# Kernel tuning notes

Hardware: AMD Instinct MI355X
Metric: run time of the kernel (lower is better)

## Reference

```python
import jax, jax.numpy as jnp
import numpy as np

NT, NP = 100000, 20000
FT, FP, H = 128, 64, 128
E, EL = 2000000, 500000
EPS = 1e-12


def _l2norm(x):
    # F.normalize(x, p=2, dim=-1): x / max(||x||, eps)
    n = jnp.sqrt(jnp.sum(x * x, axis=-1, keepdims=True))
    return x / jnp.maximum(n, EPS)


def _seg_mean(x_src, src_idx, dst_idx, n_dst, inv_cnt):
    # gather src features per edge, scatter-sum to dst, divide by in-degree
    s = jax.ops.segment_sum(x_src[src_idx], dst_idx, num_segments=n_dst)
    return s * inv_cnt[:, None]


def setup_inputs() -> dict:
    key = jax.random.key(0)
    ks = jax.random.split(key, 24)

    def w(k, fan_in, fan_out):
        return jax.random.normal(k, (fan_in, fan_out), jnp.float32) / np.sqrt(fan_in)

    inp = {
        "x_track": jax.random.normal(ks[0], (NT, FT), jnp.float32),
        "x_playlist": jax.random.normal(ks[1], (NP, FP), jnp.float32),
        "edge_src": jax.random.randint(ks[2], (E,), 0, NT),
        "edge_dst": jax.random.randint(ks[3], (E,), 0, NP),
        "label_src": jax.random.randint(ks[4], (EL,), 0, NT),
        "label_dst": jax.random.randint(ks[5], (EL,), 0, NP),
        # per-type input projections (PyG Linear, bias=True)
        "Wn_t": w(ks[6], FT, H), "bn_t": jnp.zeros((H,), jnp.float32),
        "Wn_p": w(ks[7], FP, H), "bn_p": jnp.zeros((H,), jnp.float32),
        # layer1: edge type track->playlist (dst playlist) and reverse (dst track)
        "W1_l_p": w(ks[8], H, H), "b1_p": jnp.zeros((H,), jnp.float32), "W1_r_p": w(ks[9], H, H),
        "W1_l_t": w(ks[10], H, H), "b1_t": jnp.zeros((H,), jnp.float32), "W1_r_t": w(ks[11], H, H),
        # layer2
        "W2_l_p": w(ks[12], H, H), "b2_p": jnp.zeros((H,), jnp.float32), "W2_r_p": w(ks[13], H, H),
        "W2_l_t": w(ks[14], H, H), "b2_t": jnp.zeros((H,), jnp.float32), "W2_r_t": w(ks[15], H, H),
    }
    return inp


def reference(x_track, x_playlist, edge_src, edge_dst, label_src, label_dst,
              Wn_t, bn_t, Wn_p, bn_p,
              W1_l_p, b1_p, W1_r_p, W1_l_t, b1_t, W1_r_t,
              W2_l_p, b2_p, W2_r_p, W2_l_t, b2_t, W2_r_t):
    nt, np_ = x_track.shape[0], x_playlist.shape[0]
    ones = jnp.ones(edge_src.shape, jnp.float32)
    inv_cnt_p = 1.0 / jnp.maximum(jax.ops.segment_sum(ones, edge_dst, num_segments=np_), 1.0)
    inv_cnt_t = 1.0 / jnp.maximum(jax.ops.segment_sum(ones, edge_src, num_segments=nt), 1.0)

    # per-type input linear
    h_t = x_track @ Wn_t + bn_t        # [NT, H]
    h_p = x_playlist @ Wn_p + bn_p     # [NP, H]

    # hetero SAGE layer 1 (normalize=True) + relu
    agg_p = _seg_mean(h_t, edge_src, edge_dst, np_, inv_cnt_p)  # track -> playlist
    agg_t = _seg_mean(h_p, edge_dst, edge_src, nt, inv_cnt_t)   # playlist -> track (rev edges)
    o_p = jax.nn.relu(_l2norm(agg_p @ W1_l_p + b1_p + h_p @ W1_r_p))
    o_t = jax.nn.relu(_l2norm(agg_t @ W1_l_t + b1_t + h_t @ W1_r_t))

    # hetero SAGE layer 2 (normalize=True), no relu
    agg_p2 = _seg_mean(o_t, edge_src, edge_dst, np_, inv_cnt_p)
    agg_t2 = _seg_mean(o_p, edge_dst, edge_src, nt, inv_cnt_t)
    z_p = _l2norm(agg_p2 @ W2_l_p + b2_p + o_p @ W2_r_p)
    z_t = _l2norm(agg_t2 @ W2_l_t + b2_t + o_t @ W2_r_t)

    # link predictor: dot product of endpoint embeddings
    return jnp.sum(z_t[label_src] * z_p[label_dst], axis=-1)  # [EL]
```

## Files before the change

kernel.cpp:

```cpp
#include <hip/hip_runtime.h>
#include <hip/hip_bf16.h>

#define H 128

typedef __attribute__((ext_vector_type(8))) _Float16 f16x8;
typedef __attribute__((ext_vector_type(4))) _Float16 f16x4;
typedef __attribute__((ext_vector_type(4))) float f32x4;

static inline size_t align_up(size_t x, size_t a){ return (x + a - 1) & ~(a - 1); }

__device__ inline f32x4 mfma16h(f16x8 a, f16x8 b, f32x4 c){
  return __builtin_amdgcn_mfma_f32_16x16x32_f16(a, b, c, 0, 0, 0);
}

__device__ inline void gload_lds16(const void* g, void* l){
  __builtin_amdgcn_global_load_lds(
      (const __attribute__((address_space(1))) void*)g,
      (__attribute__((address_space(3))) void*)l, 16, 0, 0);
}

__global__ __launch_bounds__(256) void hist_buckets(const int* __restrict__ src, const int* __restrict__ dst,
    int E, int* __restrict__ cnt_b_p, int* __restrict__ cnt_b_t){
  __shared__ int hp[256], ht[256];
  int tid = threadIdx.x;
  hp[tid] = 0; ht[tid] = 0;
  __syncthreads();
  for (int i = blockIdx.x * 256 + tid; i < E; i += gridDim.x * 256){
    atomicAdd(&hp[dst[i] >> 7], 1);
    atomicAdd(&ht[src[i] >> 9], 1);
  }
  __syncthreads();
  if (hp[tid]) atomicAdd(&cnt_b_p[tid], hp[tid]);
  if (ht[tid]) atomicAdd(&cnt_b_t[tid], ht[tid]);
}

__global__ void scan_buckets(const int* __restrict__ cb_p, const int* __restrict__ cb_t, int nbp, int nbt,
                             int* __restrict__ base_p, int* __restrict__ base_t,
                             int* __restrict__ cur_p, int* __restrict__ cur_t){
  if (threadIdx.x == 0){
    int s = 0;
    for (int i = 0; i < nbp; i++){ base_p[i] = s; cur_p[i] = s; s += cb_p[i]; }
    base_p[nbp] = s;
  } else if (threadIdx.x == 1){
    int s = 0;
    for (int i = 0; i < nbt; i++){ base_t[i] = s; cur_t[i] = s; s += cb_t[i]; }
    base_t[nbt] = s;
  }
}

__global__ __launch_bounds__(256) void bin_edges(const int* __restrict__ keys, const int* __restrict__ vals,
    int E, int shift, int nb, int* __restrict__ cursor, unsigned* __restrict__ rec_out){
  const int CH = 4096, IT = 16;
  __shared__ int hist[256];
  __shared__ int excl[256];
  __shared__ int gbase[256];
  __shared__ unsigned recs[CH];
  __shared__ unsigned char binid[CH];
  int tid = threadIdx.x;
  int start = blockIdx.x * CH;
  int cnt = E - start; if (cnt > CH) cnt = CH;
  if (cnt <= 0) return;
  hist[tid] = 0;
  __syncthreads();
  int b[IT]; int rank[IT]; unsigned rc[IT];
  unsigned mask = (1u << shift) - 1u;
  #pragma unroll
  for (int q = 0; q < IT; q++){
    int i = tid + q * 256;
    if (i < cnt){
      int k = keys[start + i], v = vals[start + i];
      b[q] = k >> shift;
      rc[q] = ((unsigned)v << shift) | ((unsigned)k & mask);
      rank[q] = atomicAdd(&hist[b[q]], 1);
    } else b[q] = -1;
  }
  __syncthreads();
  int lane = tid & 63, wid = tid >> 6;
  if (wid == 0){
    int h0 = hist[lane*4], h1 = hist[lane*4+1], h2 = hist[lane*4+2], h3 = hist[lane*4+3];
    int s = h0 + h1 + h2 + h3;
    int sc = s;
    #pragma unroll
    for (int o = 1; o < 64; o <<= 1){ int t = __shfl_up(sc, (unsigned)o, 64); if (lane >= o) sc += t; }
    int base = sc - s;
    excl[lane*4] = base; excl[lane*4+1] = base + h0;
    excl[lane*4+2] = base + h0 + h1; excl[lane*4+3] = base + h0 + h1 + h2;
  }
  __syncthreads();
  #pragma unroll
  for (int q = 0; q < IT; q++){
    if (b[q] >= 0){
      int pos = excl[b[q]] + rank[q];
      recs[pos] = rc[q];
      binid[pos] = (unsigned char)b[q];
    }
  }
  if (tid < nb && hist[tid] > 0) gbase[tid] = atomicAdd(&cursor[tid], hist[tid]);
  __syncthreads();
  for (int i = tid; i < cnt; i += 256){
    int bb = binid[i];
    rec_out[gbase[bb] + (i - excl[bb])] = recs[i];
  }
}

template<int LOC>
__global__ __launch_bounds__(256) void build_csr(const unsigned* __restrict__ rec, const int* __restrict__ bbase,
    int nkeys, int E, int* __restrict__ off, float* __restrict__ inv, int* __restrict__ csr){
  constexpr int LB = (LOC == 128) ? 7 : 9;
  __shared__ int hist[LOC];
  __shared__ int excl[LOC];
  __shared__ int cur[LOC];
  __shared__ int wsum[8];
  int b = blockIdx.x, tid = threadIdx.x;
  int s = bbase[b], e = bbase[b + 1];
  for (int k = tid; k < LOC; k += 256){ hist[k] = 0; cur[k] = 0; }
  __syncthreads();
  for (int i = s + tid; i < e; i += 256) atomicAdd(&hist[rec[i] & (LOC - 1)], 1);
  __syncthreads();
  int lane = tid & 63, wid = tid >> 6;
  constexpr int BPT = (LOC + 255) / 256;
  int h[BPT]; int ssum = 0;
  #pragma unroll
  for (int q = 0; q < BPT; q++){
    int k = tid * BPT + q;
    h[q] = (k < LOC) ? hist[k] : 0;
    ssum += h[q];
  }
  int sc = ssum;
  #pragma unroll
  for (int o = 1; o < 64; o <<= 1){ int t = __shfl_up(sc, (unsigned)o, 64); if (lane >= o) sc += t; }
  if (lane == 63) wsum[wid] = sc;
  __syncthreads();
  int base = 0;
  for (int w = 0; w < wid; w++) base += wsum[w];
  int ex = base + sc - ssum;
  #pragma unroll
  for (int q = 0; q < BPT; q++){
    int k = tid * BPT + q;
    if (k < LOC) excl[k] = ex;
    ex += h[q];
  }
  __syncthreads();
  int keybase = b << LB;
  for (int k = tid; k < LOC; k += 256){
    int gk = keybase + k;
    if (gk < nkeys){
      off[gk] = s + excl[k];
      int c = hist[k];
      inv[gk] = 1.0f / (float)(c > 1 ? c : 1);
    }
  }
  if (b == (int)gridDim.x - 1 && tid == 0) off[nkeys] = E;
  for (int i = s + tid; i < e; i += 256){
    unsigned r = rec[i];
    int k = (int)(r & (LOC - 1));
    int rk = atomicAdd(&cur[k], 1);
    csr[s + excl[k] + rk] = (int)(r >> LB);
  }
}

struct PackArgs {
  const float* src[10];
  _Float16* dst[10];
  int K[10];
  int start[11];
};
__global__ __launch_bounds__(256) void pack_w(PackArgs pa){
  int t = blockIdx.x * 256 + threadIdx.x;
  if (t >= pa.start[10]) return;
  int m = 0;
  #pragma unroll
  for (int i = 1; i < 10; i++) if (t >= pa.start[i]) m = i;
  int local = t - pa.start[m];
  int k = local >> 7, n = local & 127;
  float w = pa.src[m][local];
  _Float16 hi = (_Float16)w;
  _Float16 lo = (_Float16)(w - (float)hi);
  _Float16* d = pa.dst[m];
  int Km = pa.K[m];
  d[n * Km + k] = hi;
  d[128 * Km + n * Km + k] = lo;
}

template<int KA, bool CVT, bool DUAL, bool NORM, bool RELU>
__global__ __launch_bounds__(512) void sage_mfma(
    const void* __restrict__ Ain, const _Float16* __restrict__ Bs,
    const _Float16* __restrict__ WlT, const _Float16* __restrict__ WrT,
    const float* __restrict__ bias, _Float16* __restrict__ OUT, int M, int ntiles)
{
  constexpr int KST = KA / 32;
  constexpr int RB_A = CVT ? KA * 4 : KA * 2;
  constexpr int CHA = RB_A / 16;
  constexpr int NIA = 64 * CHA / 512;
  constexpr int NIB = DUAL ? 2 : 0;
  constexpr int LPI = NIA + NIB;
  constexpr int ABYTES = 64 * RB_A;
  constexpr int BBYTES = DUAL ? 64 * 256 : 0;
  constexpr int BUFB = ABYTES + BBYTES;

  __shared__ __align__(16) char lds[2 * BUFB];
  __shared__ float red[8][64];

  const int t    = threadIdx.x;
  const int wid  = t >> 6;
  const int lane = t & 63;
  const int l15  = lane & 15;
  const int lkg  = lane >> 4;
  const int colg = wid * 16 + l15;

  f16x8 wl_hi[KST], wl_lo[KST];
  {
    const _Float16* bh = WlT + (size_t)colg * KA + lkg * 8;
    #pragma unroll
    for (int ks = 0; ks < KST; ks++){
      wl_hi[ks] = *(const f16x8*)(bh + ks * 32);
      wl_lo[ks] = *(const f16x8*)(bh + 128 * KA + ks * 32);
    }
  }
  f16x8 wr_hi[DUAL ? 4 : 1], wr_lo[DUAL ? 4 : 1];
  if (DUAL){
    const _Float16* bh = WrT + (size_t)colg * 128 + lkg * 8;
    #pragma unroll
    for (int ks = 0; ks < (DUAL ? 4 : 1); ks++){
      wr_hi[ks] = *(const f16x8*)(bh + ks * 32);
      wr_lo[ks] = *(const f16x8*)(bh + 128 * 128 + ks * 32);
    }
  }
  const float bb = bias[colg];

  auto stage = [&](int tile, char* dstA, char* dstB){
    int row0 = tile * 64;
    #pragma unroll
    for (int q = 0; q < NIA; q++){
      int lc  = q * 512 + t;
      int row = lc / CHA;
      int ch  = lc - row * CHA;
      int grow = row0 + row; if (grow > M - 1) grow = M - 1;
      int gch = ch ^ (row & 7);
      gload_lds16((const char*)Ain + (size_t)grow * RB_A + gch * 16, dstA + lc * 16);
    }
    if (DUAL){
      #pragma unroll
      for (int q = 0; q < NIB; q++){
        int lc  = q * 512 + t;
        int row = lc >> 4;
        int ch  = lc & 15;
        int grow = row0 + row; if (grow > M - 1) grow = M - 1;
        int gch = ch ^ (row & 7);
        gload_lds16((const char*)Bs + (size_t)grow * 256 + gch * 16, dstB + lc * 16);
      }
    }
  };

  int p = 0;
  stage(blockIdx.x, lds, lds + ABYTES);

  for (int t0 = blockIdx.x; t0 < ntiles; t0 += gridDim.x){
    const int row0 = t0 * 64;
    const int tn = t0 + (int)gridDim.x;
    const bool hasnext = tn < ntiles;
    if (hasnext) stage(tn, lds + (p ^ 1) * BUFB, lds + (p ^ 1) * BUFB + ABYTES);

    if (hasnext){
      if constexpr (LPI == 4) asm volatile("s_waitcnt vmcnt(4)" ::: "memory");
      else                    asm volatile("s_waitcnt vmcnt(2)" ::: "memory");
    } else {
      asm volatile("s_waitcnt vmcnt(0)" ::: "memory");
    }
    __builtin_amdgcn_s_barrier();
    asm volatile("" ::: "memory");

    const char* bufA = lds + p * BUFB;
    const char* bufB = bufA + ABYTES;

    f32x4 acc[4];
    #pragma unroll
    for (int tt = 0; tt < 4; tt++){
      acc[tt] = (f32x4){0.f, 0.f, 0.f, 0.f};
      const int rl = tt * 16 + l15;
      const int sw = rl & 7;
      if (CVT){
        const char* ap = bufA + rl * RB_A;
        #pragma unroll
        for (int ks = 0; ks < KST; ks++){
          int c0 = lkg * 2 + ks * 8;
          f32x4 a0 = *(const f32x4*)(ap + ((c0    ) ^ sw) * 16);
          f32x4 a1 = *(const f32x4*)(ap + ((c0 + 1) ^ sw) * 16);
          f16x8 af;
          #pragma unroll
          for (int e = 0; e < 8; e++) af[e] = (_Float16)(e < 4 ? a0[e] : a1[e - 4]);
          acc[tt] = mfma16h(af, wl_hi[ks], acc[tt]);
          acc[tt] = mfma16h(af, wl_lo[ks], acc[tt]);
        }
      } else {
        const char* ap = bufA + rl * RB_A;
        #pragma unroll
        for (int ks = 0; ks < KST; ks++){
          f16x8 af = *(const f16x8*)(ap + ((ks * 4 + lkg) ^ sw) * 16);
          acc[tt] = mfma16h(af, wl_hi[ks], acc[tt]);
          acc[tt] = mfma16h(af, wl_lo[ks], acc[tt]);
        }
      }
      if (DUAL){
        const char* bp = bufB + rl * 256;
        #pragma unroll
        for (int ks = 0; ks < 4; ks++){
          f16x8 bf = *(const f16x8*)(bp + ((ks * 4 + lkg) ^ sw) * 16);
          acc[tt] = mfma16h(bf, wr_hi[ks], acc[tt]);
          acc[tt] = mfma16h(bf, wr_lo[ks], acc[tt]);
        }
      }
      acc[tt].x += bb; acc[tt].y += bb; acc[tt].z += bb; acc[tt].w += bb;
    }

    if (NORM){
      #pragma unroll
      for (int tt = 0; tt < 4; tt++){
        #pragma unroll
        for (int r = 0; r < 4; r++){
          float v = acc[tt][r] * acc[tt][r];
          v += __shfl_xor(v, 1, 64);
          v += __shfl_xor(v, 2, 64);
          v += __shfl_xor(v, 4, 64);
          v += __shfl_xor(v, 8, 64);
          if (l15 == 0) red[wid][tt * 16 + lkg * 4 + r] = v;
        }
      }
      asm volatile("s_waitcnt lgkmcnt(0)" ::: "memory");
      __builtin_amdgcn_s_barrier();
      asm volatile("" ::: "memory");
      #pragma unroll
      for (int tt = 0; tt < 4; tt++){
        #pragma unroll
        for (int r = 0; r < 4; r++){
          int idx = tt * 16 + lkg * 4 + r;
          float s = 0.f;
          #pragma unroll
          for (int w2 = 0; w2 < 8; w2++) s += red[w2][idx];
          float scale = 1.f / fmaxf(sqrtf(s), 1e-12f);
          acc[tt][r] *= scale;
        }
      }
    }
    if (RELU){
      #pragma unroll
      for (int tt = 0; tt < 4; tt++){
        acc[tt].x = fmaxf(acc[tt].x, 0.f); acc[tt].y = fmaxf(acc[tt].y, 0.f);
        acc[tt].z = fmaxf(acc[tt].z, 0.f); acc[tt].w = fmaxf(acc[tt].w, 0.f);
      }
    }
    #pragma unroll
    for (int tt = 0; tt < 4; tt++){
      #pragma unroll
      for (int r = 0; r < 4; r++){
        int row = row0 + tt * 16 + lkg * 4 + r;
        if (row < M) OUT[(size_t)row * H + colg] = (_Float16)acc[tt][r];
      }
    }
    if (!NORM){
      asm volatile("s_waitcnt lgkmcnt(0)" ::: "memory");
      __builtin_amdgcn_s_barrier();
      asm volatile("" ::: "memory");
    }
    p ^= 1;
  }
}

struct SageJob {
  const _Float16* A;
  const _Float16* Bs;
  const _Float16* WlT;
  const _Float16* WrT;
  const float* bias;
  _Float16* OUT;
  int M;
  int ntiles;
  int nblk;
};
template<bool RELU>
__global__ __launch_bounds__(512) void sage_mfma2(SageJob j0, SageJob j1){
  constexpr int KST = 4;
  constexpr int RB_A = 256;
  constexpr int CHA = 16;
  constexpr int NIA = 2, NIB = 2;
  constexpr int ABYTES = 64 * 256;
  constexpr int BUFB = 2 * ABYTES;

  __shared__ __align__(16) char lds[2 * BUFB];
  __shared__ float red[8][64];

  const bool second = (int)blockIdx.x >= j0.nblk;
  const SageJob j = second ? j1 : j0;
  const int bid = (int)blockIdx.x - (second ? j0.nblk : 0);
  const int M = j.M, ntiles = j.ntiles, nblk = j.nblk;

  const int t    = threadIdx.x;
  const int wid  = t >> 6;
  const int lane = t & 63;
  const int l15  = lane & 15;
  const int lkg  = lane >> 4;
  const int colg = wid * 16 + l15;

  f16x8 wl_hi[KST], wl_lo[KST], wr_hi[KST], wr_lo[KST];
  {
    const _Float16* bh = j.WlT + (size_t)colg * 128 + lkg * 8;
    const _Float16* bh2 = j.WrT + (size_t)colg * 128 + lkg * 8;
    #pragma unroll
    for (int ks = 0; ks < KST; ks++){
      wl_hi[ks] = *(const f16x8*)(bh + ks * 32);
      wl_lo[ks] = *(const f16x8*)(bh + 128 * 128 + ks * 32);
      wr_hi[ks] = *(const f16x8*)(bh2 + ks * 32);
      wr_lo[ks] = *(const f16x8*)(bh2 + 128 * 128 + ks * 32);
    }
  }
  const float bb = j.bias[colg];

  auto stage = [&](int tile, char* dstA, char* dstB){
    int row0 = tile * 64;
    #pragma unroll
    for (int q = 0; q < NIA; q++){
      int lc  = q * 512 + t;
      int row = lc / CHA;
      int ch  = lc - row * CHA;
      int grow = row0 + row; if (grow > M - 1) grow = M - 1;
      int gch = ch ^ (row & 7);
      gload_lds16((const char*)j.A + (size_t)grow * 256 + gch * 16, dstA + lc * 16);
    }
    #pragma unroll
    for (int q = 0; q < NIB; q++){
      int lc  = q * 512 + t;
      int row = lc >> 4;
      int ch  = lc & 15;
      int grow = row0 + row; if (grow > M - 1) grow = M - 1;
      int gch = ch ^ (row & 7);
      gload_lds16((const char*)j.Bs + (size_t)grow * 256 + gch * 16, dstB + lc * 16);
    }
  };

  int p = 0;
  if (bid < ntiles) stage(bid, lds, lds + ABYTES);

  for (int t0 = bid; t0 < ntiles; t0 += nblk){
    const int row0 = t0 * 64;
    const int tn = t0 + nblk;
    const bool hasnext = tn < ntiles;
    if (hasnext) stage(tn, lds + (p ^ 1) * BUFB, lds + (p ^ 1) * BUFB + ABYTES);

    if (hasnext) asm volatile("s_waitcnt vmcnt(4)" ::: "memory");
    else         asm volatile("s_waitcnt vmcnt(0)" ::: "memory");
    __builtin_amdgcn_s_barrier();
    asm volatile("" ::: "memory");

    const char* bufA = lds + p * BUFB;
    const char* bufB = bufA + ABYTES;

    f32x4 acc[4];
    #pragma unroll
    for (int tt = 0; tt < 4; tt++){
      acc[tt] = (f32x4){0.f, 0.f, 0.f, 0.f};
      const int rl = tt * 16 + l15;
      const int sw = rl & 7;
      const char* ap = bufA + rl * 256;
      #pragma unroll
      for (int ks = 0; ks < KST; ks++){
        f16x8 af = *(const f16x8*)(ap + ((ks * 4 + lkg) ^ sw) * 16);
        acc[tt] = mfma16h(af, wl_hi[ks], acc[tt]);
        acc[tt] = mfma16h(af, wl_lo[ks], acc[tt]);
      }
      const char* bp = bufB + rl * 256;
      #pragma unroll
      for (int ks = 0; ks < KST; ks++){
        f16x8 bf = *(const f16x8*)(bp + ((ks * 4 + lkg) ^ sw) * 16);
        acc[tt] = mfma16h(bf, wr_hi[ks], acc[tt]);
        acc[tt] = mfma16h(bf, wr_lo[ks], acc[tt]);
      }
      acc[tt].x += bb; acc[tt].y += bb; acc[tt].z += bb; acc[tt].w += bb;
    }

    #pragma unroll
    for (int tt = 0; tt < 4; tt++){
      #pragma unroll
      for (int r = 0; r < 4; r++){
        float v = acc[tt][r] * acc[tt][r];
        v += __shfl_xor(v, 1, 64);
        v += __shfl_xor(v, 2, 64);
        v += __shfl_xor(v, 4, 64);
        v += __shfl_xor(v, 8, 64);
        if (l15 == 0) red[wid][tt * 16 + lkg * 4 + r] = v;
      }
    }
    asm volatile("s_waitcnt lgkmcnt(0)" ::: "memory");
    __builtin_amdgcn_s_barrier();
    asm volatile("" ::: "memory");
    #pragma unroll
    for (int tt = 0; tt < 4; tt++){
      #pragma unroll
      for (int r = 0; r < 4; r++){
        int idx = tt * 16 + lkg * 4 + r;
        float s = 0.f;
        #pragma unroll
        for (int w2 = 0; w2 < 8; w2++) s += red[w2][idx];
        float scale = 1.f / fmaxf(sqrtf(s), 1e-12f);
        float v = acc[tt][r] * scale;
        if (RELU) v = fmaxf(v, 0.f);
        acc[tt][r] = v;
      }
    }
    #pragma unroll
    for (int tt = 0; tt < 4; tt++){
      #pragma unroll
      for (int r = 0; r < 4; r++){
        int row = row0 + tt * 16 + lkg * 4 + r;
        if (row < M) j.OUT[(size_t)row * H + colg] = (_Float16)acc[tt][r];
      }
    }
    p ^= 1;
  }
}

struct AggJob {
  const _Float16* feat;
  const int* csr;
  const int* off;
  const float* inv;
  _Float16* out;
  int n;
  int nblk;
};
__global__ __launch_bounds__(256) void agg2_kernel(AggJob j0, AggJob j1){
  const bool second = (int)blockIdx.x >= j0.nblk;
  const AggJob j = second ? j1 : j0;
  const int bid = (int)blockIdx.x - (second ? j0.nblk : 0);
  int g = bid * 16 + (threadIdx.x >> 4);
  int l = threadIdx.x & 15;
  if (g >= j.n) return;
  int s = j.off[g], e = j.off[g + 1];
  float c0[8], c1[8], c2[8], c3[8];
  #pragma unroll
  for (int q = 0; q < 8; q++){ c0[q] = 0.f; c1[q] = 0.f; c2[q] = 0.f; c3[q] = 0.f; }
  const _Float16* F = j.feat;
  int i = s;
  for (; i + 3 < e; i += 4){
    f16x8 v0 = *(const f16x8*)(F + (size_t)j.csr[i]     * H + l * 8);
    f16x8 v1 = *(const f16x8*)(F + (size_t)j.csr[i + 1] * H + l * 8);
    f16x8 v2 = *(const f16x8*)(F + (size_t)j.csr[i + 2] * H + l * 8);
    f16x8 v3 = *(const f16x8*)(F + (size_t)j.csr[i + 3] * H + l * 8);
    #pragma unroll
    for (int q = 0; q < 8; q++){
      c0[q] += (float)v0[q]; c1[q] += (float)v1[q];
      c2[q] += (float)v2[q]; c3[q] += (float)v3[q];
    }
  }
  for (; i < e; i++){
    f16x8 v0 = *(const f16x8*)(F + (size_t)j.csr[i] * H + l * 8);
    #pragma unroll
    for (int q = 0; q < 8; q++) c0[q] += (float)v0[q];
  }
  float iv = j.inv[g];
  f16x8 ov;
  #pragma unroll
  for (int q = 0; q < 8; q++){
    float r = (c0[q] + c1[q]) + (c2[q] + c3[q]);
    ov[q] = (_Float16)(r * iv);
  }
  *(f16x8*)(j.out + (size_t)g * H + l * 8) = ov;
}

__global__ __launch_bounds__(256) void dot_kernel(const _Float16* __restrict__ zt, const _Float16* __restrict__ zp,
                           const int* __restrict__ ls, const int* __restrict__ ld,
                           float* __restrict__ out, int n){
  int w = (blockIdx.x * 256 + threadIdx.x) >> 4;
  int l = threadIdx.x & 15;
  if (w >= n) return;
  f16x8 x = *(const f16x8*)&zt[(size_t)ls[w] * H + l * 8];
  f16x8 y = *(const f16x8*)&zp[(size_t)ld[w] * H + l * 8];
  float v = 0.f;
  #pragma unroll
  for (int q = 0; q < 8; q++) v += (float)x[q] * (float)y[q];
  v += __shfl_xor(v, 1, 64);
  v += __shfl_xor(v, 2, 64);
  v += __shfl_xor(v, 4, 64);
  v += __shfl_xor(v, 8, 64);
  if (l == 0) out[w] = v;
}

extern "C" void kernel_launch(void* const* d_in, const int* in_sizes, int n_in,
                              void* d_out, int out_size, void* d_ws, size_t ws_size,
                              hipStream_t stream){
  const float* x_t  = (const float*)d_in[0];
  const float* x_p  = (const float*)d_in[1];
  const int*   esrc = (const int*)d_in[2];
  const int*   edst = (const int*)d_in[3];
  const int*   lsrc = (const int*)d_in[4];
  const int*   ldst = (const int*)d_in[5];
  const float* Wn_t = (const float*)d_in[6];
  const float* bn_t = (const float*)d_in[7];
  const float* Wn_p = (const float*)d_in[8];
  const float* bn_p = (const float*)d_in[9];
  const float* W1_l_p=(const float*)d_in[10]; const float* b1_p=(const float*)d_in[11]; const float* W1_r_p=(const float*)d_in[12];
  const float* W1_l_t=(const float*)d_in[13]; const float* b1_t=(const float*)d_in[14]; const float* W1_r_t=(const float*)d_in[15];
  const float* W2_l_p=(const float*)d_in[16]; const float* b2_p=(const float*)d_in[17]; const float* W2_r_p=(const float*)d_in[18];
  const float* W2_l_t=(const float*)d_in[19]; const float* b2_t=(const float*)d_in[20]; const float* W2_r_t=(const float*)d_in[21];
  float* out = (float*)d_out;

  const int FT = 128, FP = 64;
  int NT = in_sizes[0] / FT;
  int NP = in_sizes[1] / FP;
  int E  = in_sizes[2];
  int EL = in_sizes[4];

  const int SH_P = 7, SH_T = 9;
  int nb_p = (NP + (1 << SH_P) - 1) >> SH_P;
  int nb_t = (NT + (1 << SH_T) - 1) >> SH_T;

  char* base = (char*)d_ws;
  size_t o = 0;
  auto alloc = [&](size_t bytes) -> char* { char* p = base + o; o = align_up(o + bytes, 256); return p; };
  int*   cb_p  = (int*)alloc(256 * 4);
  int*   cb_t  = (int*)alloc(256 * 4);
  size_t zero_bytes = o;
  int*   bb_p  = (int*)alloc(260 * 4);
  int*   bb_t  = (int*)alloc(260 * 4);
  int*   cu_p  = (int*)alloc(256 * 4);
  int*   cu_t  = (int*)alloc(256 * 4);
  int*   off_p = (int*)alloc((size_t)(NP + 1) * 4);
  int*   off_t = (int*)alloc((size_t)(NT + 1) * 4);
  float* inv_p = (float*)alloc((size_t)NP * 4);
  float* inv_t = (float*)alloc((size_t)NT * 4);
  unsigned* rec_p = (unsigned*)alloc((size_t)E * 4);
  unsigned* rec_t = (unsigned*)alloc((size_t)E * 4);
  int*   csr_p = (int*)alloc((size_t)E * 4);
  int*   csr_t = (int*)alloc((size_t)E * 4);
  _Float16* h_t = (_Float16*)alloc((size_t)NT * H * 2);
  _Float16* h_p = (_Float16*)alloc((size_t)NP * H * 2);
  _Float16* a_t = (_Float16*)alloc((size_t)NT * H * 2);
  _Float16* a_p = (_Float16*)alloc((size_t)NP * H * 2);

  PackArgs pa;
  const float* wsrc[10] = {Wn_t, Wn_p, W1_l_p, W1_r_p, W1_l_t, W1_r_t, W2_l_p, W2_r_p, W2_l_t, W2_r_t};
  int Ks[10] = {128, 64, 128, 128, 128, 128, 128, 128, 128, 128};
  _Float16* wpk[10];
  int st = 0;
  for (int m = 0; m < 10; m++){
    wpk[m] = (_Float16*)alloc((size_t)2 * 128 * Ks[m] * 2);
    pa.src[m] = wsrc[m]; pa.dst[m] = wpk[m]; pa.K[m] = Ks[m]; pa.start[m] = st;
    st += Ks[m] * 128;
  }
  pa.start[10] = st;
  (void)ws_size; (void)n_in; (void)out_size;

  hipMemsetAsync(base, 0, zero_bytes, stream);
  pack_w<<<(st + 255) / 256, 256, 0, stream>>>(pa);

  hist_buckets<<<512, 256, 0, stream>>>(esrc, edst, E, cb_p, cb_t);
  scan_buckets<<<1, 64, 0, stream>>>(cb_p, cb_t, nb_p, nb_t, bb_p, bb_t, cu_p, cu_t);
  int nchunks = (E + 4095) / 4096;
  bin_edges<<<nchunks, 256, 0, stream>>>(edst, esrc, E, SH_P, nb_p, cu_p, rec_p);
  bin_edges<<<nchunks, 256, 0, stream>>>(esrc, edst, E, SH_T, nb_t, cu_t, rec_t);
  build_csr<128><<<nb_p, 256, 0, stream>>>(rec_p, bb_p, NP, E, off_p, inv_p, csr_p);
  build_csr<512><<<nb_t, 256, 0, stream>>>(rec_t, bb_t, NT, E, off_t, inv_t, csr_t);

  int tiles_t = (NT + 63) / 64;
  int tiles_p = (NP + 63) / 64;
  int grid_t = tiles_t < 512 ? tiles_t : 512;
  int grid_p = tiles_p < 512 ? tiles_p : 512;

  sage_mfma<128,true,false,false,false><<<grid_t, 512, 0, stream>>>(x_t, nullptr, wpk[0], nullptr, bn_t, h_t, NT, tiles_t);
  sage_mfma<64, true,false,false,false><<<grid_p, 512, 0, stream>>>(x_p, nullptr, wpk[1], nullptr, bn_p, h_p, NP, tiles_p);

  int ablk_p = (NP + 15) / 16;
  int ablk_t = (NT + 15) / 16;
  AggJob aj_p1{h_t, csr_p, off_p, inv_p, a_p, NP, ablk_p};
  AggJob aj_t1{h_p, csr_t, off_t, inv_t, a_t, NT, ablk_t};
  AggJob aj_p2{a_t, csr_p, off_p, inv_p, h_p, NP, ablk_p};
  AggJob aj_t2{a_p, csr_t, off_t, inv_t, h_t, NT, ablk_t};

  int nblk_p = tiles_p < 96 ? tiles_p : 96;
  int nblk_t = tiles_t < 416 ? tiles_t : 416;
  SageJob sj1p{a_p, h_p, wpk[2], wpk[3], b1_p, a_p, NP, tiles_p, nblk_p};
  SageJob sj1t{a_t, h_t, wpk[4], wpk[5], b1_t, a_t, NT, tiles_t, nblk_t};
  SageJob sj2p{h_p, a_p, wpk[6], wpk[7], b2_p, h_p, NP, tiles_p, nblk_p};
  SageJob sj2t{h_t, a_t, wpk[8], wpk[9], b2_t, h_t, NT, tiles_t, nblk_t};

  agg2_kernel<<<ablk_p + ablk_t, 256, 0, stream>>>(aj_p1, aj_t1);
  sage_mfma2<true><<<nblk_p + nblk_t, 512, 0, stream>>>(sj1p, sj1t);

  agg2_kernel<<<ablk_p + ablk_t, 256, 0, stream>>>(aj_p2, aj_t2);
  sage_mfma2<false><<<nblk_p + nblk_t, 512, 0, stream>>>(sj2p, sj2t);

  dot_kernel<<<(EL + 15) / 16, 256, 0, stream>>>(h_t, h_p, lsrc, ldst, out, EL);
}
```

Baseline: 546.6 us.

## Merge preprocessing and projection kernels into fewer combined launches

```diff
diff --git a/kernel.cpp b/kernel.cpp
--- a/kernel.cpp
+++ b/kernel.cpp
@@ -4,7 +4,6 @@
 #define H 128
 
 typedef __attribute__((ext_vector_type(8))) _Float16 f16x8;
-typedef __attribute__((ext_vector_type(4))) _Float16 f16x4;
 typedef __attribute__((ext_vector_type(4))) float f32x4;
 
 static inline size_t align_up(size_t x, size_t a){ return (x + a - 1) & ~(a - 1); }
@@ -19,19 +18,45 @@
       (__attribute__((address_space(3))) void*)l, 16, 0, 0);
 }
 
-__global__ __launch_bounds__(256) void hist_buckets(const int* __restrict__ src, const int* __restrict__ dst,
-    int E, int* __restrict__ cnt_b_p, int* __restrict__ cnt_b_t){
-  __shared__ int hp[256], ht[256];
-  int tid = threadIdx.x;
-  hp[tid] = 0; ht[tid] = 0;
-  __syncthreads();
-  for (int i = blockIdx.x * 256 + tid; i < E; i += gridDim.x * 256){
-    atomicAdd(&hp[dst[i] >> 7], 1);
-    atomicAdd(&ht[src[i] >> 9], 1);
-  }
-  __syncthreads();
-  if (hp[tid]) atomicAdd(&cnt_b_p[tid], hp[tid]);
-  if (ht[tid]) atomicAdd(&cnt_b_t[tid], ht[tid]);
+struct PackArgs {
+  const float* src[10];
+  _Float16* dst[10];
+  int K[10];
+  int start[11];
+};
+
+__global__ __launch_bounds__(256) void pack_hist(PackArgs pa, int nblk_pack,
+    const int* __restrict__ src, const int* __restrict__ dst, int E,
+    int* __restrict__ cnt_b_p, int* __restrict__ cnt_b_t, int histgrid){
+  if ((int)blockIdx.x < nblk_pack){
+    int t = blockIdx.x * 256 + threadIdx.x;
+    if (t >= pa.start[10]) return;
+    int m = 0;
+    #pragma unroll
+    for (int i = 1; i < 10; i++) if (t >= pa.start[i]) m = i;
+    int local = t - pa.start[m];
+    int k = local >> 7, n = local & 127;
+    float w = pa.src[m][local];
+    _Float16 hi = (_Float16)w;
+    _Float16 lo = (_Float16)(w - (float)hi);
+    _Float16* d = pa.dst[m];
+    int Km = pa.K[m];
+    d[n * Km + k] = hi;
+    d[128 * Km + n * Km + k] = lo;
+  } else {
+    int bid = (int)blockIdx.x - nblk_pack;
+    __shared__ int hp[256], ht[256];
+    int tid = threadIdx.x;
+    hp[tid] = 0; ht[tid] = 0;
+    __syncthreads();
+    for (int i = bid * 256 + tid; i < E; i += histgrid * 256){
+      atomicAdd(&hp[dst[i] >> 7], 1);
+      atomicAdd(&ht[src[i] >> 9], 1);
+    }
+    __syncthreads();
+    if (hp[tid]) atomicAdd(&cnt_b_p[tid], hp[tid]);
+    if (ht[tid]) atomicAdd(&cnt_b_t[tid], ht[tid]);
+  }
 }
 
 __global__ void scan_buckets(const int* __restrict__ cb_p, const int* __restrict__ cb_t, int nbp, int nbt,
@@ -48,16 +73,12 @@
   }
 }
 
-__global__ __launch_bounds__(256) void bin_edges(const int* __restrict__ keys, const int* __restrict__ vals,
-    int E, int shift, int nb, int* __restrict__ cursor, unsigned* __restrict__ rec_out){
+__device__ inline void bin_body(const int* __restrict__ keys, const int* __restrict__ vals,
+    int E, int shift, int nb, int* __restrict__ cursor, unsigned* __restrict__ rec_out, int chunk,
+    int* hist, int* excl, int* gbase, unsigned* recs, unsigned char* binid){
   const int CH = 4096, IT = 16;
-  __shared__ int hist[256];
-  __shared__ int excl[256];
-  __shared__ int gbase[256];
-  __shared__ unsigned recs[CH];
-  __shared__ unsigned char binid[CH];
   int tid = threadIdx.x;
-  int start = blockIdx.x * CH;
+  int start = chunk * CH;
   int cnt = E - start; if (cnt > CH) cnt = CH;
   if (cnt <= 0) return;
   hist[tid] = 0;
@@ -103,15 +124,24 @@
   }
 }
 
-template<int LOC>
-__global__ __launch_bounds__(256) void build_csr(const unsigned* __restrict__ rec, const int* __restrict__ bbase,
-    int nkeys, int E, int* __restrict__ off, float* __restrict__ inv, int* __restrict__ csr){
-  constexpr int LB = (LOC == 128) ? 7 : 9;
-  __shared__ int hist[LOC];
-  __shared__ int excl[LOC];
-  __shared__ int cur[LOC];
-  __shared__ int wsum[8];
-  int b = blockIdx.x, tid = threadIdx.x;
+__global__ __launch_bounds__(256) void bin2(const int* __restrict__ esrc, const int* __restrict__ edst,
+    int E, int nb_p, int* cu_p, unsigned* rec_p, int nb_t, int* cu_t, unsigned* rec_t, int nchunks){
+  __shared__ int hist[256];
+  __shared__ int excl[256];
+  __shared__ int gbase[256];
+  __shared__ unsigned recs[4096];
+  __shared__ unsigned char binid[4096];
+  if ((int)blockIdx.x < nchunks)
+    bin_body(edst, esrc, E, 7, nb_p, cu_p, rec_p, blockIdx.x, hist, excl, gbase, recs, binid);
+  else
+    bin_body(esrc, edst, E, 9, nb_t, cu_t, rec_t, blockIdx.x - nchunks, hist, excl, gbase, recs, binid);
+}
+
+template<int LOC, int LB>
+__device__ inline void build_body(const unsigned* __restrict__ rec, const int* __restrict__ bbase,
+    int nkeys, int E, int* __restrict__ off, float* __restrict__ inv, int* __restrict__ csr,
+    int b, int nb, int* hist, int* excl, int* cur, int* wsum){
+  int tid = threadIdx.x;
   int s = bbase[b], e = bbase[b + 1];
   for (int k = tid; k < LOC; k += 256){ hist[k] = 0; cur[k] = 0; }
   __syncthreads();
@@ -150,7 +180,7 @@
       inv[gk] = 1.0f / (float)(c > 1 ? c : 1);
     }
   }
-  if (b == (int)gridDim.x - 1 && tid == 0) off[nkeys] = E;
+  if (b == nb - 1 && tid == 0) off[nkeys] = E;
   for (int i = s + tid; i < e; i += 256){
     unsigned r = rec[i];
     int k = (int)(r & (LOC - 1));
@@ -159,47 +189,35 @@
   }
 }
 
-struct PackArgs {
-  const float* src[10];
-  _Float16* dst[10];
-  int K[10];
-  int start[11];
+__global__ __launch_bounds__(256) void build2(
+    const unsigned* rec_p, const int* bb_p, int NPk, int* off_p, float* inv_p, int* csr_p, int nb_p,
+    const unsigned* rec_t, const int* bb_t, int NTk, int* off_t, float* inv_t, int* csr_t, int nb_t, int E){
+  __shared__ int hist[512];
+  __shared__ int excl[512];
+  __shared__ int cur[512];
+  __shared__ int wsum[8];
+  if ((int)blockIdx.x < nb_p)
+    build_body<128,7>(rec_p, bb_p, NPk, E, off_p, inv_p, csr_p, blockIdx.x, nb_p, hist, excl, cur, wsum);
+  else
+    build_body<512,9>(rec_t, bb_t, NTk, E, off_t, inv_t, csr_t, blockIdx.x - nb_p, nb_t, hist, excl, cur, wsum);
+}
+
+struct ProjJob {
+  const float* A;
+  const _Float16* WT;
+  const float* bias;
+  _Float16* OUT;
+  int M;
+  int ntiles;
+  int nblk;
 };
-__global__ __launch_bounds__(256) void pack_w(PackArgs pa){
-  int t = blockIdx.x * 256 + threadIdx.x;
-  if (t >= pa.start[10]) return;
-  int m = 0;
-  #pragma unroll
-  for (int i = 1; i < 10; i++) if (t >= pa.start[i]) m = i;
-  int local = t - pa.start[m];
-  int k = local >> 7, n = local & 127;
-  float w = pa.src[m][local];
-  _Float16 hi = (_Float16)w;
-  _Float16 lo = (_Float16)(w - (float)hi);
-  _Float16* d = pa.dst[m];
-  int Km = pa.K[m];
-  d[n * Km + k] = hi;
-  d[128 * Km + n * Km + k] = lo;
-}
-
-template<int KA, bool CVT, bool DUAL, bool NORM, bool RELU>
-__global__ __launch_bounds__(512) void sage_mfma(
-    const void* __restrict__ Ain, const _Float16* __restrict__ Bs,
-    const _Float16* __restrict__ WlT, const _Float16* __restrict__ WrT,
-    const float* __restrict__ bias, _Float16* __restrict__ OUT, int M, int ntiles)
-{
+template<int KA>
+__device__ inline void proj_body(ProjJob j, int bid, char* lds){
   constexpr int KST = KA / 32;
-  constexpr int RB_A = CVT ? KA * 4 : KA * 2;
+  constexpr int RB_A = KA * 4;
   constexpr int CHA = RB_A / 16;
   constexpr int NIA = 64 * CHA / 512;
-  constexpr int NIB = DUAL ? 2 : 0;
-  constexpr int LPI = NIA + NIB;
   constexpr int ABYTES = 64 * RB_A;
-  constexpr int BBYTES = DUAL ? 64 * 256 : 0;
-  constexpr int BUFB = ABYTES + BBYTES;
-
-  __shared__ __align__(16) char lds[2 * BUFB];
-  __shared__ float red[8][64];
 
   const int t    = threadIdx.x;
   const int wid  = t >> 6;
@@ -207,28 +225,20 @@
   const int l15  = lane & 15;
   const int lkg  = lane >> 4;
   const int colg = wid * 16 + l15;
+  const int M = j.M, ntiles = j.ntiles, nblk = j.nblk;
 
   f16x8 wl_hi[KST], wl_lo[KST];
   {
-    const _Float16* bh = WlT + (size_t)colg * KA + lkg * 8;
+    const _Float16* bh = j.WT + (size_t)colg * KA + lkg * 8;
     #pragma unroll
     for (int ks = 0; ks < KST; ks++){
       wl_hi[ks] = *(const f16x8*)(bh + ks * 32);
       wl_lo[ks] = *(const f16x8*)(bh + 128 * KA + ks * 32);
     }
   }
-  f16x8 wr_hi[DUAL ? 4 : 1], wr_lo[DUAL ? 4 : 1];
-  if (DUAL){
-    const _Float16* bh = WrT + (size_t)colg * 128 + lkg * 8;
-    #pragma unroll
-    for (int ks = 0; ks < (DUAL ? 4 : 1); ks++){
-      wr_hi[ks] = *(const f16x8*)(bh + ks * 32);
-      wr_lo[ks] = *(const f16x8*)(bh + 128 * 128 + ks * 32);
-    }
-  }
-  const float bb = bias[colg];
-
-  auto stage = [&](int tile, char* dstA, char* dstB){
+  const float bb = j.bias[colg];
+
+  auto stage = [&](int tile, char* dstA){
     int row0 = tile * 64;
     #pragma unroll
     for (int q = 0; q < NIA; q++){
@@ -237,32 +247,21 @@
       int ch  = lc - row * CHA;
       int grow = row0 + row; if (grow > M - 1) grow = M - 1;
       int gch = ch ^ (row & 7);
-      gload_lds16((const char*)Ain + (size_t)grow * RB_A + gch * 16, dstA + lc * 16);
-    }
-    if (DUAL){
-      #pragma unroll
-      for (int q = 0; q < NIB; q++){
-        int lc  = q * 512 + t;
-        int row = lc >> 4;
-        int ch  = lc & 15;
-        int grow = row0 + row; if (grow > M - 1) grow = M - 1;
-        int gch = ch ^ (row & 7);
-        gload_lds16((const char*)Bs + (size_t)grow * 256 + gch * 16, dstB + lc * 16);
-      }
+      gload_lds16((const char*)j.A + (size_t)grow * RB_A + gch * 16, dstA + lc * 16);
     }
   };
 
   int p = 0;
-  stage(blockIdx.x, lds, lds + ABYTES);
-
-  for (int t0 = blockIdx.x; t0 < ntiles; t0 += gridDim.x){
+  if (bid < ntiles) stage(bid, lds);
+
+  for (int t0 = bid; t0 < ntiles; t0 += nblk){
     const int row0 = t0 * 64;
-    const int tn = t0 + (int)gridDim.x;
+    const int tn = t0 + nblk;
     const bool hasnext = tn < ntiles;
-    if (hasnext) stage(tn, lds + (p ^ 1) * BUFB, lds + (p ^ 1) * BUFB + ABYTES);
+    if (hasnext) stage(tn, lds + (p ^ 1) * ABYTES);
 
     if (hasnext){
-      if constexpr (LPI == 4) asm volatile("s_waitcnt vmcnt(4)" ::: "memory");
+      if constexpr (NIA == 4) asm volatile("s_waitcnt vmcnt(4)" ::: "memory");
       else                    asm volatile("s_waitcnt vmcnt(2)" ::: "memory");
     } else {
       asm volatile("s_waitcnt vmcnt(0)" ::: "memory");
@@ -270,8 +269,7 @@
     __builtin_amdgcn_s_barrier();
     asm volatile("" ::: "memory");
 
-    const char* bufA = lds + p * BUFB;
-    const char* bufB = bufA + ABYTES;
+    const char* bufA = lds + p * ABYTES;
 
     f32x4 acc[4];
     #pragma unroll
@@ -279,91 +277,39 @@
       acc[tt] = (f32x4){0.f, 0.f, 0.f, 0.f};
       const int rl = tt * 16 + l15;
       const int sw = rl & 7;
-      if (CVT){
-        const char* ap = bufA + rl * RB_A;
+      const char* ap = bufA + rl * RB_A;
+      #pragma unroll
+      for (int ks = 0; ks < KST; ks++){
+        int c0 = lkg * 2 + ks * 8;
+        f32x4 a0 = *(const f32x4*)(ap + ((c0    ) ^ sw) * 16);
+        f32x4 a1 = *(const f32x4*)(ap + ((c0 + 1) ^ sw) * 16);
+        f16x8 af;
         #pragma unroll
-        for (int ks = 0; ks < KST; ks++){
-          int c0 = lkg * 2 + ks * 8;
-          f32x4 a0 = *(const f32x4*)(ap + ((c0    ) ^ sw) * 16);
-          f32x4 a1 = *(const f32x4*)(ap + ((c0 + 1) ^ sw) * 16);
-          f16x8 af;
-          #pragma unroll
-          for (int e = 0; e < 8; e++) af[e] = (_Float16)(e < 4 ? a0[e] : a1[e - 4]);
-          acc[tt] = mfma16h(af, wl_hi[ks], acc[tt]);
-          acc[tt] = mfma16h(af, wl_lo[ks], acc[tt]);
-        }
-      } else {
-        const char* ap = bufA + rl * RB_A;
-        #pragma unroll
-        for (int ks = 0; ks < KST; ks++){
-          f16x8 af = *(const f16x8*)(ap + ((ks * 4 + lkg) ^ sw) * 16);
-          acc[tt] = mfma16h(af, wl_hi[ks], acc[tt]);
-          acc[tt] = mfma16h(af, wl_lo[ks], acc[tt]);
-        }
-      }
-      if (DUAL){
-        const char* bp = bufB + rl * 256;
-        #pragma unroll
-        for (int ks = 0; ks < 4; ks++){
-          f16x8 bf = *(const f16x8*)(bp + ((ks * 4 + lkg) ^ sw) * 16);
-          acc[tt] = mfma16h(bf, wr_hi[ks], acc[tt]);
-          acc[tt] = mfma16h(bf, wr_lo[ks], acc[tt]);
-        }
+        for (int e = 0; e < 8; e++) af[e] = (_Float16)(e < 4 ? a0[e] : a1[e - 4]);
+        acc[tt] = mfma16h(af, wl_hi[ks], acc[tt]);
+        acc[tt] = mfma16h(af, wl_lo[ks], acc[tt]);
       }
       acc[tt].x += bb; acc[tt].y += bb; acc[tt].z += bb; acc[tt].w += bb;
     }
 
-    if (NORM){
-      #pragma unroll
-      for (int tt = 0; tt < 4; tt++){
-        #pragma unroll
-        for (int r = 0; r < 4; r++){
-          float v = acc[tt][r] * acc[tt][r];
-          v += __shfl_xor(v, 1, 64);
-          v += __shfl_xor(v, 2, 64);
-          v += __shfl_xor(v, 4, 64);
-          v += __shfl_xor(v, 8, 64);
-          if (l15 == 0) red[wid][tt * 16 + lkg * 4 + r] = v;
-        }
-      }
-      asm volatile("s_waitcnt lgkmcnt(0)" ::: "memory");
-      __builtin_amdgcn_s_barrier();
-      asm volatile("" ::: "memory");
-      #pragma unroll
-      for (int tt = 0; tt < 4; tt++){
-        #pragma unroll
-        for (int r = 0; r < 4; r++){
-          int idx = tt * 16 + lkg * 4 + r;
-          float s = 0.f;
-          #pragma unroll
-          for (int w2 = 0; w2 < 8; w2++) s += red[w2][idx];
-          float scale = 1.f / fmaxf(sqrtf(s), 1e-12f);
-          acc[tt][r] *= scale;
-        }
-      }
-    }
-    if (RELU){
-      #pragma unroll
-      for (int tt = 0; tt < 4; tt++){
-        acc[tt].x = fmaxf(acc[tt].x, 0.f); acc[tt].y = fmaxf(acc[tt].y, 0.f);
-        acc[tt].z = fmaxf(acc[tt].z, 0.f); acc[tt].w = fmaxf(acc[tt].w, 0.f);
-      }
-    }
     #pragma unroll
     for (int tt = 0; tt < 4; tt++){
       #pragma unroll
       for (int r = 0; r < 4; r++){
         int row = row0 + tt * 16 + lkg * 4 + r;
-        if (row < M) OUT[(size_t)row * H + colg] = (_Float16)acc[tt][r];
+        if (row < M) j.OUT[(size_t)row * H + colg] = (_Float16)acc[tt][r];
       }
     }
-    if (!NORM){
-      asm volatile("s_waitcnt lgkmcnt(0)" ::: "memory");
-      __builtin_amdgcn_s_barrier();
-      asm volatile("" ::: "memory");
-    }
+    asm volatile("s_waitcnt lgkmcnt(0)" ::: "memory");
+    __builtin_amdgcn_s_barrier();
+    asm volatile("" ::: "memory");
     p ^= 1;
   }
+}
+__global__ __launch_bounds__(512) void proj2(ProjJob jt, ProjJob jp){
+  __shared__ __align__(16) char lds[2 * 64 * 512];
+  if ((int)blockIdx.x < jt.nblk) proj_body<128>(jt, blockIdx.x, lds);
+  else                           proj_body<64>(jp, (int)blockIdx.x - jt.nblk, lds);
 }
 
 struct SageJob {
@@ -380,7 +326,6 @@
 template<bool RELU>
 __global__ __launch_bounds__(512) void sage_mfma2(SageJob j0, SageJob j1){
   constexpr int KST = 4;
-  constexpr int RB_A = 256;
   constexpr int CHA = 16;
   constexpr int NIA = 2, NIB = 2;
   constexpr int ABYTES = 64 * 256;
@@ -650,23 +595,23 @@
   (void)ws_size; (void)n_in; (void)out_size;
 
   hipMemsetAsync(base, 0, zero_bytes, stream);
-  pack_w<<<(st + 255) / 256, 256, 0, stream>>>(pa);
-
-  hist_buckets<<<512, 256, 0, stream>>>(esrc, edst, E, cb_p, cb_t);
+
+  int nblk_pack = (st + 255) / 256;
+  const int histgrid = 512;
+  pack_hist<<<nblk_pack + histgrid, 256, 0, stream>>>(pa, nblk_pack, esrc, edst, E, cb_p, cb_t, histgrid);
   scan_buckets<<<1, 64, 0, stream>>>(cb_p, cb_t, nb_p, nb_t, bb_p, bb_t, cu_p, cu_t);
   int nchunks = (E + 4095) / 4096;
-  bin_edges<<<nchunks, 256, 0, stream>>>(edst, esrc, E, SH_P, nb_p, cu_p, rec_p);
-  bin_edges<<<nchunks, 256, 0, stream>>>(esrc, edst, E, SH_T, nb_t, cu_t, rec_t);
-  build_csr<128><<<nb_p, 256, 0, stream>>>(rec_p, bb_p, NP, E, off_p, inv_p, csr_p);
-  build_csr<512><<<nb_t, 256, 0, stream>>>(rec_t, bb_t, NT, E, off_t, inv_t, csr_t);
+  bin2<<<2 * nchunks, 256, 0, stream>>>(esrc, edst, E, nb_p, cu_p, rec_p, nb_t, cu_t, rec_t, nchunks);
+  build2<<<nb_p + nb_t, 256, 0, stream>>>(rec_p, bb_p, NP, off_p, inv_p, csr_p, nb_p,
+                                          rec_t, bb_t, NT, off_t, inv_t, csr_t, nb_t, E);
 
   int tiles_t = (NT + 63) / 64;
   int tiles_p = (NP + 63) / 64;
-  int grid_t = tiles_t < 512 ? tiles_t : 512;
-  int grid_p = tiles_p < 512 ? tiles_p : 512;
-
-  sage_mfma<128,true,false,false,false><<<grid_t, 512, 0, stream>>>(x_t, nullptr, wpk[0], nullptr, bn_t, h_t, NT, tiles_t);
-  sage_mfma<64, true,false,false,false><<<grid_p, 512, 0, stream>>>(x_p, nullptr, wpk[1], nullptr, bn_p, h_p, NP, tiles_p);
+  int pblk_t = tiles_t < 448 ? tiles_t : 448;
+  int pblk_p = tiles_p < 64 ? tiles_p : 64;
+  ProjJob pjt{x_t, wpk[0], bn_t, h_t, NT, tiles_t, pblk_t};
+  ProjJob pjp{x_p, wpk[1], bn_p, h_p, NP, tiles_p, pblk_p};
+  proj2<<<pblk_t + pblk_p, 512, 0, stream>>>(pjt, pjp);
 
   int ablk_p = (NP + 15) / 16;
   int ablk_t = (NT + 15) / 16;
```

Result: faster. 505.8 us (-7.5%).
